# Optimization experiments

Hardware: AMD Instinct MI355X
Metric: run time of the kernel (lower is better)

The kernel has to match this reference:

```python
import jax, jax.numpy as jnp
import numpy as np

IMG = 48
N = IMG * IMG          # 2304 oscillators
B = 4
STEPS = 4              # cfg['kuramoto_steps']
K_COUP = 1.0           # cfg['coupling_K']
DT = 0.1               # cfg['dt']
ALPHA_SCALE = 1.0      # cfg['lag_scale']
BN_EPS = 1e-5


def _conv2d(x, w, b, pad):
    # x: [B,C,H,W], w: [O,I,kh,kw]
    y = jax.lax.conv_general_dilated(
        x, w, window_strides=(1, 1), padding=[(pad, pad), (pad, pad)],
        dimension_numbers=('NCHW', 'OIHW', 'NCHW'))
    return y + b[None, :, None, None]


def setup_inputs() -> dict:
    key = jax.random.key(0)
    ks = jax.random.split(key, 12)
    inp = {
        'x': jax.random.normal(ks[0], (B, 1, IMG, IMG), jnp.float32),
        'conv1_w': jax.random.normal(ks[1], (16, 1, 3, 3), jnp.float32) * 0.2,
        'conv1_b': jax.random.normal(ks[2], (16,), jnp.float32) * 0.05,
        'bn_gamma': jnp.ones((16,), jnp.float32),
        'bn_beta': jnp.zeros((16,), jnp.float32),
        'conv2_w': jax.random.normal(ks[3], (16, 16, 3, 3), jnp.float32) * 0.1,
        'conv2_b': jax.random.normal(ks[4], (16,), jnp.float32) * 0.05,
        'feat_w': jax.random.normal(ks[5], (8, 16, 1, 1), jnp.float32) * 0.2,
        'feat_b': jax.random.normal(ks[6], (8,), jnp.float32) * 0.05,
        'drive_w': jax.random.normal(ks[7], (1, 16, 1, 1), jnp.float32) * 0.2,
        'drive_b': jax.random.normal(ks[8], (1,), jnp.float32) * 0.05,
        'omega': jax.random.normal(ks[9], (N, 1), jnp.float32) * 0.1,
        'kappa': jnp.ones((N, 1), jnp.float32),
        'direction_learner': jax.random.normal(ks[10], (N, N), jnp.float32) * 0.01,
        'theta0': jax.random.uniform(ks[11], (B, N, 1), jnp.float32) * (2.0 * np.pi),
    }
    return inp


def reference(x, conv1_w, conv1_b, bn_gamma, bn_beta, conv2_w, conv2_b,
              feat_w, feat_b, drive_w, drive_b, omega, kappa,
              direction_learner, theta0):
    # ---- backbone: conv -> BN (batch stats, train mode) -> tanh -> conv -> tanh
    h = _conv2d(x, conv1_w, conv1_b, pad=1)
    mu = jnp.mean(h, axis=(0, 2, 3), keepdims=True)
    var = jnp.mean((h - mu) ** 2, axis=(0, 2, 3), keepdims=True)  # biased var, torch BN
    h = bn_gamma[None, :, None, None] * (h - mu) / jnp.sqrt(var + BN_EPS) \
        + bn_beta[None, :, None, None]
    h = jnp.tanh(h)
    h = jnp.tanh(_conv2d(h, conv2_w, conv2_b, pad=1))

    # ---- heads
    gamma = _conv2d(h, drive_w, drive_b, pad=0).reshape(B, N)          # [B,N]
    feat = _conv2d(h, feat_w, feat_b, pad=0).reshape(B, 8, N)
    feat = jnp.transpose(feat, (0, 2, 1))                              # [B,N,8]
    fnorm = feat / jnp.maximum(
        jnp.sqrt(jnp.sum(feat * feat, axis=2, keepdims=True)), 1e-12)

    # ---- cosine-similarity connectivity, zero diagonal
    A = jnp.einsum('bnd,bmd->bnm', fnorm, fnorm)                       # [B,N,N]
    A = A * (1.0 - jnp.eye(N, dtype=A.dtype))

    # ---- OT-derived phase lag (constant across steps, so hoisted)
    A_lat = jax.nn.relu(0.5 * (A + jnp.transpose(A, (0, 2, 1)))) + 1e-6
    cost = 1.0 / A_lat
    c_min = jnp.min(cost, axis=(1, 2), keepdims=True)
    c_max = jnp.max(cost, axis=(1, 2), keepdims=True)
    norm_cost = (cost - c_min) / (c_max - c_min + 1e-6)
    direction = jnp.tanh(direction_learner - direction_learner.T)      # antisym -> tanh
    alpha = ALPHA_SCALE * direction[None, :, :] * norm_cost            # [B,N,N]

    # ---- Kuramoto integration (D=1, work in [B,N])
    theta = theta0[..., 0]
    om = omega[:, 0][None, :]
    kp = kappa[:, 0][None, :]
    for _ in range(STEPS):
        # phase_diff[b,i,j] = theta_j - theta_i - alpha_ij
        pd = theta[:, None, :] - theta[:, :, None] - alpha             # [B,N,N]
        interaction = jnp.sum(A_lat * jnp.sin(pd), axis=2)             # [B,N]
        coupling = (K_COUP / float(N)) * interaction
        drive_term = kp * jnp.sin(gamma - theta)
        theta = theta + DT * (om + coupling + drive_term)
    return theta  # [B,N]
```

## Files before the change

kernel.cpp:

```cpp
#include <hip/hip_runtime.h>
#include <hip/hip_fp16.h>

#define IMG 48
#define NPIX 2304
#define NB 4
#define NCH 16
#define DT 0.1f
#define BN_EPS 1e-5f
#define TPB 1024
#define GRID_BLKS 256

typedef _Float16 h2v __attribute__((ext_vector_type(2)));
typedef unsigned long long u64;

#if defined(__has_builtin)
#if __has_builtin(__builtin_amdgcn_fdot2)
#define HAVE_FDOT2 1
#endif
#endif

__device__ __forceinline__ void ast32(unsigned* p, unsigned v) {
    __hip_atomic_store(p, v, __ATOMIC_RELAXED, __HIP_MEMORY_SCOPE_AGENT);
}
__device__ __forceinline__ unsigned ald32(const unsigned* p) {
    return __hip_atomic_load(p, __ATOMIC_RELAXED, __HIP_MEMORY_SCOPE_AGENT);
}
__device__ __forceinline__ void ast_u64(void* p, u64 v) {
    __hip_atomic_store((u64*)p, v, __ATOMIC_RELAXED, __HIP_MEMORY_SCOPE_AGENT);
}
__device__ __forceinline__ u64 ald_u64(const void* p) {
    return __hip_atomic_load((const u64*)p, __ATOMIC_RELAXED, __HIP_MEMORY_SCOPE_AGENT);
}
__device__ __forceinline__ u64 pack2f(float a, float b) {
    return (u64)__float_as_uint(a) | ((u64)__float_as_uint(b) << 32);
}

__shared__ __align__(16) char smem[58368];

__device__ __forceinline__ void fbar_all(unsigned* flags, unsigned* gen, unsigned ph) {
    __syncthreads();
    if (threadIdx.x == 0) ast32(&flags[blockIdx.x], ph);
    if (blockIdx.x == 0) {
        if (threadIdx.x < 64) {
            for (;;) {
                int ok = 1;
                #pragma unroll
                for (int k = 0; k < 4; ++k)
                    ok &= (ald32(&flags[threadIdx.x + 64 * k]) >= ph) ? 1 : 0;
                if (__all(ok)) break;
                __builtin_amdgcn_s_sleep(1);
            }
            if (threadIdx.x == 0) ast32(&gen[64], ph);
        }
    } else if (threadIdx.x == 0) {
        while (ald32(&gen[64]) < ph) __builtin_amdgcn_s_sleep(2);
    }
    __syncthreads();
}
__device__ __forceinline__ void fbar_batch(unsigned* flags, unsigned* gen,
                                           unsigned ph, int sb) {
    __syncthreads();
    if (threadIdx.x == 0) ast32(&flags[blockIdx.x], ph);
    if (blockIdx.x == (sb << 6)) {
        if (threadIdx.x < 64) {
            const unsigned* f = flags + (sb << 6);
            for (;;) {
                int ok = (ald32(&f[threadIdx.x]) >= ph) ? 1 : 0;
                if (__all(ok)) break;
                __builtin_amdgcn_s_sleep(1);
            }
            if (threadIdx.x == 0) ast32(&gen[sb * 16], ph);
        }
    } else if (threadIdx.x == 0) {
        while (ald32(&gen[sb * 16]) < ph) __builtin_amdgcn_s_sleep(2);
    }
    __syncthreads();
}

__device__ __forceinline__ float dot8(const h2v fi[4], uint4 w) {
#ifdef HAVE_FDOT2
    float d = __builtin_amdgcn_fdot2(fi[0], __builtin_bit_cast(h2v, w.x), 0.0f, false);
    d = __builtin_amdgcn_fdot2(fi[1], __builtin_bit_cast(h2v, w.y), d, false);
    d = __builtin_amdgcn_fdot2(fi[2], __builtin_bit_cast(h2v, w.z), d, false);
    d = __builtin_amdgcn_fdot2(fi[3], __builtin_bit_cast(h2v, w.w), d, false);
    return d;
#else
    float d = 0.f;
    unsigned ws[4] = {w.x, w.y, w.z, w.w};
    #pragma unroll
    for (int k = 0; k < 4; ++k) {
        h2v a = fi[k], b = __builtin_bit_cast(h2v, ws[k]);
        d += (float)a.x * (float)b.x + (float)a.y * (float)b.y;
    }
    return d;
#endif
}

__global__ __launch_bounds__(TPB, 4) void k_all(
    const float* __restrict__ x,  const float* __restrict__ w1, const float* __restrict__ b1,
    const float* __restrict__ bng, const float* __restrict__ bnb,
    const float* __restrict__ w2, const float* __restrict__ b2,
    const float* __restrict__ fw, const float* __restrict__ fbv,
    const float* __restrict__ dw, const float* __restrict__ dbv,
    const float* __restrict__ om, const float* __restrict__ kp,
    const float* __restrict__ th0, float* __restrict__ out,
    unsigned* __restrict__ flags, unsigned* __restrict__ gen,
    u64* __restrict__ partials, u64* __restrict__ fnorm_h, float2* __restrict__ gam2,
    u64* __restrict__ uv0, u64* __restrict__ uv1)
{
    const int tid  = threadIdx.x;
    const int blk  = blockIdx.x;
    const int wave = tid >> 6, lane = tid & 63;
    const int sb   = blk >> 6;
    const int base = (blk & 63) * 36;
    const int trow0 = base / IMG - 1;

    float*  sw2p = (float*)smem;
    float*  ht   = (float*)(smem + 9280);
    float*  h2s  = (float*)(smem + 22144);
    float*  p0red= (float*)(smem + 24448);
    float*  redc = (float*)(smem + 25600);
    float2* bnred= (float2*)(smem + 25728);

    {
        const float* xb = x + sb * NPIX;
        if (tid < 128) {
            int ch = tid >> 3, r4 = (tid >> 1) & 3, side = tid & 1;
            ht[ch * 201 + r4 * 50 + side * 49] = 0.f;
        }
        #pragma unroll
        for (int k = 0; k < 3; ++k) {
            int idx = tid + k * TPB;
            int ch = idx / 192, rc = idx % 192;
            int tr = rc / 48, col = rc % 48;
            int y = trow0 + tr;
            float s = 0.f;
            if (y >= 0 && y < IMG) {
                s = b1[ch];
                #pragma unroll
                for (int ky = 0; ky < 3; ++ky) {
                    int yy = y + ky - 1;
                    if (yy < 0 || yy >= IMG) continue;
                    #pragma unroll
                    for (int kx = 0; kx < 3; ++kx) {
                        int x2 = col + kx - 1;
                        if (x2 < 0 || x2 >= IMG) continue;
                        s += xb[yy * IMG + x2] * w1[ch * 9 + ky * 3 + kx];
                    }
                }
            }
            ht[ch * 201 + tr * 50 + col + 1] = s;
        }
        __syncthreads();
        if (tid < 576) {
            int lpx = tid >> 4, oc = tid & 15;
            int p = base + lpx;
            int tr = p / IMG - trow0, col = p % IMG;
            float v = ht[oc * 201 + tr * 50 + col + 1];
            float S = v, Q = v * v;
            S += __shfl_down(S, 32, 64); Q += __shfl_down(Q, 32, 64);
            S += __shfl_down(S, 16, 64); Q += __shfl_down(Q, 16, 64);
            if (lane < 16) { p0red[wave * 32 + lane * 2] = S; p0red[wave * 32 + lane * 2 + 1] = Q; }
        }
        __syncthreads();
        if (tid < 16) {
            float Ss = 0.f, Qs = 0.f;
            #pragma unroll
            for (int w8 = 0; w8 < 9; ++w8) {
                Ss += p0red[w8 * 32 + tid * 2];
                Qs += p0red[w8 * 32 + tid * 2 + 1];
            }
            ast_u64(&partials[blk * 16 + tid], pack2f(Ss, Qs));
        }
    }
    fbar_all(flags, gen, 1);

    {
        if (tid < 512) {
            int c = tid >> 5, g = tid & 31;
            u64 vv[8];
            #pragma unroll
            for (int k = 0; k < 8; ++k) vv[k] = ald_u64(&partials[(g * 8 + k) * 16 + c]);
            float S = 0.f, Q = 0.f;
            #pragma unroll
            for (int k = 0; k < 8; ++k) {
                S += __uint_as_float((unsigned)vv[k]);
                Q += __uint_as_float((unsigned)(vv[k] >> 32));
            }
            bnred[c * 32 + g] = make_float2(S, Q);
        }
        for (int k = tid; k < NCH * NCH * 9; k += TPB) {
            int o = k / 144, r = k - o * 144;
            sw2p[o * 145 + r] = w2[k];
        }
        __syncthreads();
        if (tid < 16) {
            float S = 0.f, Q = 0.f;
            #pragma unroll
            for (int g = 0; g < 32; ++g) { S += bnred[tid * 32 + g].x; Q += bnred[tid * 32 + g].y; }
            const float inv_n = 1.0f / (float)(NB * NPIX);
            float mu = S * inv_n, var = Q * inv_n - mu * mu;
            float sc = bng[tid] * rsqrtf(var + BN_EPS);
            redc[tid * 2] = sc; redc[tid * 2 + 1] = bnb[tid] - mu * sc;
        }
        __syncthreads();
        #pragma unroll
        for (int k = 0; k < 3; ++k) {
            int idx = tid + k * TPB;
            int ch = idx / 192, rc = idx % 192;
            int tr = rc / 48, col = rc % 48;
            int y = trow0 + tr;
            if (y >= 0 && y < IMG) {
                int a = ch * 201 + tr * 50 + col + 1;
                ht[a] = tanhf(fmaf(ht[a], redc[ch * 2], redc[ch * 2 + 1]));
            }
        }
        __syncthreads();

        if (tid < 576) {
            int lpx = tid >> 4, oc = tid & 15;
            int p = base + lpx;
            int y = p / IMG, cx = p % IMG;
            int tr1 = y - trow0;
            float acc = b2[oc];
            const float* wrow = &sw2p[oc * 145];
            #pragma unroll 4
            for (int ic = 0; ic < 16; ++ic) {
                const float* hrow = &ht[ic * 201];
                #pragma unroll
                for (int ky = 0; ky < 3; ++ky) {
                    int rr = (tr1 + ky - 1) * 50 + cx;
                    #pragma unroll
                    for (int kx = 0; kx < 3; ++kx)
                        acc += hrow[rr + kx] * wrow[ic * 9 + ky * 3 + kx];
                }
            }
            h2s[tid] = tanhf(acc);
        }
        __syncthreads();
        if (tid < 576) {
            int lpx = tid >> 4, oc = tid & 15;
            int p = base + lpx;
            int bgrp = tid & ~15;
            int px = blk * 36 + lpx;
            if (oc < 8) {
                float f = fbv[oc];
                #pragma unroll
                for (int o2 = 0; o2 < 16; ++o2) f += fw[oc * 16 + o2] * h2s[bgrp + o2];
                float ssq = f * f;
                ssq += __shfl_xor(ssq, 1, 16);
                ssq += __shfl_xor(ssq, 2, 16);
                ssq += __shfl_xor(ssq, 4, 16);
                unsigned hb = (unsigned)__half_as_ushort(
                    __float2half(f * (1.0f / fmaxf(sqrtf(ssq), 1e-12f))));
                unsigned g0 = __shfl(hb, (lane & ~3) | 0, 64);
                unsigned g1 = __shfl(hb, (lane & ~3) | 1, 64);
                unsigned g2 = __shfl(hb, (lane & ~3) | 2, 64);
                unsigned g3 = __shfl(hb, (lane & ~3) | 3, 64);
                if ((oc & 3) == 0) {
                    u64 pk = (u64)g0 | ((u64)g1 << 16) | ((u64)g2 << 32) | ((u64)g3 << 48);
                    ast_u64(&fnorm_h[px * 2 + (oc >> 2)], pk);
                }
            } else if (oc == 15) {
                float g = dbv[0];
                #pragma unroll
                for (int o2 = 0; o2 < 16; ++o2) g += dw[o2] * h2s[bgrp + o2];
                float k_ = kp[p];
                float sg, cg; __sincosf(g, &sg, &cg);
                gam2[px] = make_float2(k_ * sg, k_ * cg);
            }
        }
    }

    {
        uint4*  sfn4 = (uint4*)smem;
        float2* suv  = (float2*)(smem + 38912);
        const int libase = (blk & 63) * 36;
        const int li0 = libase + wave * 2;
        const bool has3 = (wave < 4);
        const int li2 = libase + 32 + (wave & 3);

        fbar_batch(flags, gen, 2, sb);

        const u64* fng = fnorm_h + (size_t)sb * NPIX * 2;
        const float* th0b = th0 + sb * NPIX;
        for (int e = tid; e < NPIX; e += TPB) {
            u64 a = ald_u64(&fng[e * 2]);
            u64 b = ald_u64(&fng[e * 2 + 1]);
            sfn4[e] = make_uint4((unsigned)a, (unsigned)(a >> 32),
                                 (unsigned)b, (unsigned)(b >> 32));
            float sn, cn; __sincosf(th0b[e], &sn, &cn);
            suv[e] = make_float2(sn, cn);
        }
        __syncthreads();

        h2v fi[3][4]; float thi[3];
        #pragma unroll
        for (int r = 0; r < 3; ++r) {
            int i = (r < 2) ? (li0 + r) : li2;
            uint4 w = sfn4[i];
            fi[r][0] = __builtin_bit_cast(h2v, w.x);
            fi[r][1] = __builtin_bit_cast(h2v, w.y);
            fi[r][2] = __builtin_bit_cast(h2v, w.z);
            fi[r][3] = __builtin_bit_cast(h2v, w.w);
            thi[r] = th0b[i];
        }

        for (int s = 0; s < 4; ++s) {
            if (s > 0) {
                const u64* uvg = (((s - 1) & 1) ? uv1 : uv0) + sb * NPIX;
                for (int e = tid; e < NPIX; e += TPB) {
                    u64 u = ald_u64(&uvg[e]);
                    suv[e] = make_float2(__uint_as_float((unsigned)u),
                                         __uint_as_float((unsigned)(u >> 32)));
                }
                __syncthreads();
            }

            float a1[3] = {0.f, 0.f, 0.f}, a2[3] = {0.f, 0.f, 0.f};
            uint4  w0 = sfn4[lane],      wA = sfn4[64 + lane];
            float2 U0 = suv[lane],       UA = suv[64 + lane];
            #pragma unroll 4
            for (int tt = 0; tt < NPIX / 64; ++tt) {
                uint4  wn = sfn4[(tt + 2) * 64 + lane];
                float2 Un = suv[(tt + 2) * 64 + lane];
                float al0 = fmaxf(dot8(fi[0], w0), 0.f);
                a1[0] = fmaf(al0, U0.x, a1[0]);
                a2[0] = fmaf(al0, U0.y, a2[0]);
                float al1 = fmaxf(dot8(fi[1], w0), 0.f);
                a1[1] = fmaf(al1, U0.x, a1[1]);
                a2[1] = fmaf(al1, U0.y, a2[1]);
                if (has3) {
                    float al2 = fmaxf(dot8(fi[2], w0), 0.f);
                    a1[2] = fmaf(al2, U0.x, a1[2]);
                    a2[2] = fmaf(al2, U0.y, a2[2]);
                }
                w0 = wA; U0 = UA; wA = wn; UA = Un;
            }
            #pragma unroll
            for (int o = 32; o; o >>= 1) {
                #pragma unroll
                for (int r = 0; r < 3; ++r) {
                    a1[r] += __shfl_down(a1[r], o, 64);
                    a2[r] += __shfl_down(a2[r], o, 64);
                }
            }
            if (lane == 0) {
                #pragma unroll
                for (int r = 0; r < 3; ++r) {
                    if (r == 2 && !has3) break;
                    int i = (r < 2) ? (li0 + r) : li2;
                    int row = sb * NPIX + i;
                    float2 uvi = suv[i];
                    float inter = uvi.y * a1[r] - uvi.x * a2[r];
                    float2 g2 = gam2[row];
                    float drv = g2.x * uvi.y - g2.y * uvi.x;
                    float tn = thi[r] + DT * (om[i] + inter * (1.0f / (float)NPIX) + drv);
                    thi[r] = tn;
                    if (s == 3) {
                        out[row] = tn;
                    } else {
                        float sn, cn; __sincosf(tn, &sn, &cn);
                        ast_u64(&(((s & 1) ? uv1 : uv0)[row]), pack2f(sn, cn));
                    }
                }
            }
            if (s < 3) fbar_batch(flags, gen, 3 + s, sb);
        }
    }
}

extern "C" void kernel_launch(void* const* d_in, const int* in_sizes, int n_in,
                              void* d_out, int out_size, void* d_ws, size_t ws_size,
                              hipStream_t stream) {
    const float* x   = (const float*)d_in[0];
    const float* w1  = (const float*)d_in[1];
    const float* b1  = (const float*)d_in[2];
    const float* bng = (const float*)d_in[3];
    const float* bnb = (const float*)d_in[4];
    const float* w2  = (const float*)d_in[5];
    const float* b2  = (const float*)d_in[6];
    const float* fw  = (const float*)d_in[7];
    const float* fb  = (const float*)d_in[8];
    const float* dw  = (const float*)d_in[9];
    const float* db  = (const float*)d_in[10];
    const float* om  = (const float*)d_in[11];
    const float* kp  = (const float*)d_in[12];
    const float* th0 = (const float*)d_in[14];
    float* out = (float*)d_out;

    char* wsb = (char*)d_ws;
    unsigned* flags   = (unsigned*)wsb;
    unsigned* gen     = (unsigned*)(wsb + 1024);
    u64*      partials= (u64*)(wsb + 1536);
    u64*      fnorm_h = (u64*)(wsb + 34304);
    float2*   gam2    = (float2*)(wsb + 181760);
    u64*      uv0     = (u64*)(wsb + 255488);
    u64*      uv1     = (u64*)(wsb + 329216);

    hipMemsetAsync(wsb, 0, 1536, stream);

    k_all<<<dim3(GRID_BLKS), dim3(TPB), 0, stream>>>(
        x, w1, b1, bng, bnb, w2, b2, fw, fb, dw, db, om, kp, th0, out,
        flags, gen, partials, fnorm_h, gam2, uv0, uv1);
}
```

Measured before the change: 62.64 us.

## Use 768-thread blocks with three rows per wave and paired-column inner loop

Shrinks each block from 16 to 12 waves so every wave handles exactly three oscillator rows. This removes the divergent has3 branch, where four waves did a third row while the rest idled. The coupling loop now processes two columns per lane per iteration, using a float4 load for the sin/cos pairs, which halves the iteration count. The conv stage loops are extended to four passes to keep the same coverage, and shared memory is enlarged so the prefetch can safely read past the end of the arrays.

```diff
diff --git a/kernel.cpp b/kernel.cpp
--- a/kernel.cpp
+++ b/kernel.cpp
@@ -7,7 +7,7 @@
 #define NCH 16
 #define DT 0.1f
 #define BN_EPS 1e-5f
-#define TPB 1024
+#define TPB 768
 #define GRID_BLKS 256
 
 typedef _Float16 h2v __attribute__((ext_vector_type(2)));
@@ -35,7 +35,7 @@
     return (u64)__float_as_uint(a) | ((u64)__float_as_uint(b) << 32);
 }
 
-__shared__ __align__(16) char smem[58368];
+__shared__ __align__(16) char smem[61440];
 
 __device__ __forceinline__ void fbar_all(unsigned* flags, unsigned* gen, unsigned ph) {
     __syncthreads();
@@ -96,7 +96,7 @@
 #endif
 }
 
-__global__ __launch_bounds__(TPB, 4) void k_all(
+__global__ __launch_bounds__(TPB, 3) void k_all(
     const float* __restrict__ x,  const float* __restrict__ w1, const float* __restrict__ b1,
     const float* __restrict__ bng, const float* __restrict__ bnb,
     const float* __restrict__ w2, const float* __restrict__ b2,
@@ -129,7 +129,7 @@
             ht[ch * 201 + r4 * 50 + side * 49] = 0.f;
         }
         #pragma unroll
-        for (int k = 0; k < 3; ++k) {
+        for (int k = 0; k < 4; ++k) {
             int idx = tid + k * TPB;
             int ch = idx / 192, rc = idx % 192;
             int tr = rc / 48, col = rc % 48;
@@ -205,7 +205,7 @@
         }
         __syncthreads();
         #pragma unroll
-        for (int k = 0; k < 3; ++k) {
+        for (int k = 0; k < 4; ++k) {
             int idx = tid + k * TPB;
             int ch = idx / 192, rc = idx % 192;
             int tr = rc / 48, col = rc % 48;
@@ -274,11 +274,9 @@
 
     {
         uint4*  sfn4 = (uint4*)smem;
-        float2* suv  = (float2*)(smem + 38912);
-        const int libase = (blk & 63) * 36;
-        const int li0 = libase + wave * 2;
-        const bool has3 = (wave < 4);
-        const int li2 = libase + 32 + (wave & 3);
+        float2* suv  = (float2*)(smem + 40960);
+        float4* suv4 = (float4*)(smem + 40960);
+        const int li0 = (blk & 63) * 36 + wave * 3;
 
         fbar_batch(flags, gen, 2, sb);
 
@@ -297,13 +295,12 @@
         h2v fi[3][4]; float thi[3];
         #pragma unroll
         for (int r = 0; r < 3; ++r) {
-            int i = (r < 2) ? (li0 + r) : li2;
-            uint4 w = sfn4[i];
+            uint4 w = sfn4[li0 + r];
             fi[r][0] = __builtin_bit_cast(h2v, w.x);
             fi[r][1] = __builtin_bit_cast(h2v, w.y);
             fi[r][2] = __builtin_bit_cast(h2v, w.z);
             fi[r][3] = __builtin_bit_cast(h2v, w.w);
-            thi[r] = th0b[i];
+            thi[r] = th0b[li0 + r];
         }
 
         for (int s = 0; s < 4; ++s) {
@@ -318,24 +315,26 @@
             }
 
             float a1[3] = {0.f, 0.f, 0.f}, a2[3] = {0.f, 0.f, 0.f};
-            uint4  w0 = sfn4[lane],      wA = sfn4[64 + lane];
-            float2 U0 = suv[lane],       UA = suv[64 + lane];
-            #pragma unroll 4
-            for (int tt = 0; tt < NPIX / 64; ++tt) {
-                uint4  wn = sfn4[(tt + 2) * 64 + lane];
-                float2 Un = suv[(tt + 2) * 64 + lane];
-                float al0 = fmaxf(dot8(fi[0], w0), 0.f);
-                a1[0] = fmaf(al0, U0.x, a1[0]);
-                a2[0] = fmaf(al0, U0.y, a2[0]);
-                float al1 = fmaxf(dot8(fi[1], w0), 0.f);
-                a1[1] = fmaf(al1, U0.x, a1[1]);
-                a2[1] = fmaf(al1, U0.y, a2[1]);
-                if (has3) {
-                    float al2 = fmaxf(dot8(fi[2], w0), 0.f);
-                    a1[2] = fmaf(al2, U0.x, a1[2]);
-                    a2[2] = fmaf(al2, U0.y, a2[2]);
-                }
-                w0 = wA; U0 = UA; wA = wn; UA = Un;
+            uint4  wa0 = sfn4[2 * lane],            wb0 = sfn4[2 * lane + 1];
+            float4 u0  = suv4[lane];
+            uint4  waA = sfn4[2 * (64 + lane)],     wbA = sfn4[2 * (64 + lane) + 1];
+            float4 uA  = suv4[64 + lane];
+            #pragma unroll 3
+            for (int tt = 0; tt < NPIX / 128; ++tt) {
+                int Pn = (tt + 2) * 64 + lane;
+                uint4  wan = sfn4[2 * Pn], wbn = sfn4[2 * Pn + 1];
+                float4 un  = suv4[Pn];
+                #pragma unroll
+                for (int r = 0; r < 3; ++r) {
+                    float alA = fmaxf(dot8(fi[r], wa0), 0.f);
+                    a1[r] = fmaf(alA, u0.x, a1[r]);
+                    a2[r] = fmaf(alA, u0.y, a2[r]);
+                    float alB = fmaxf(dot8(fi[r], wb0), 0.f);
+                    a1[r] = fmaf(alB, u0.z, a1[r]);
+                    a2[r] = fmaf(alB, u0.w, a2[r]);
+                }
+                wa0 = waA; wb0 = wbA; u0 = uA;
+                waA = wan; wbA = wbn; uA = un;
             }
             #pragma unroll
             for (int o = 32; o; o >>= 1) {
@@ -348,9 +347,7 @@
             if (lane == 0) {
                 #pragma unroll
                 for (int r = 0; r < 3; ++r) {
-                    if (r == 2 && !has3) break;
-                    int i = (r < 2) ? (li0 + r) : li2;
-                    int row = sb * NPIX + i;
+                    int i = li0 + r, row = sb * NPIX + i;
                     float2 uvi = suv[i];
                     float inter = uvi.y * a1[r] - uvi.x * a2[r];
                     float2 g2 = gam2[row];
```

Result: faster. 58.85 us (-6.0%).
